# Optimization experiments

Measured on AMD Instinct MI355X. Metric: run time of the kernel, lower is better.

Reference implementation:

```python
import jax, jax.numpy as jnp
import numpy as np

B, N, K, E, H, V = 128, 256, 4, 300, 150, 32000  # batch, nodes/tree, max children, embed, hidden, vocab
DELTA = 1.0


def setup_inputs() -> dict:
    key = jax.random.key(0)
    ks = jax.random.split(key, 8)
    query = jax.random.randint(ks[0], (B, N), 0, V, dtype=jnp.int32)
    pos = jax.random.randint(ks[1], (B, N), 0, V, dtype=jnp.int32)
    neg = jax.random.randint(ks[2], (B, N), 0, V, dtype=jnp.int32)
    # Complete K-ary tree over N nodes: children of node t are {K*t+1, ..., K*t+K} < N; root = node 0.
    ch = np.full((N, K), -1, dtype=np.int32)
    for t in range(N):
        for j in range(K):
            c = K * t + 1 + j
            if c < N:
                ch[t, j] = c
    children = jnp.asarray(ch)
    emb = jax.random.normal(ks[3], (V, E), dtype=jnp.float32) * 0.02
    W_iou = jax.random.normal(ks[4], (E, 3 * H), dtype=jnp.float32) * 0.05
    U_iou = jax.random.normal(ks[5], (H, 3 * H), dtype=jnp.float32) * 0.05
    b_iou = jnp.zeros((3 * H,), jnp.float32)
    W_f = jax.random.normal(ks[6], (E, H), dtype=jnp.float32) * 0.05
    U_f = jax.random.normal(ks[7], (H, H), dtype=jnp.float32) * 0.05
    b_f = jnp.zeros((H,), jnp.float32)
    return {"query": query, "pos": pos, "neg": neg, "children": children,
            "emb": emb, "W_iou": W_iou, "U_iou": U_iou, "b_iou": b_iou,
            "W_f": W_f, "U_f": U_f, "b_f": b_f}


def _childsum_treelstm(x, children, W_iou, U_iou, b_iou, W_f, U_f, b_f):
    """x: [B, N, E] node embeddings. Returns root (c, h): each [B, H]."""
    Bn, Nn, _ = x.shape
    Hh = U_f.shape[0]
    h0 = jnp.zeros((Bn, Nn, Hh), x.dtype)
    c0 = jnp.zeros((Bn, Nn, Hh), x.dtype)

    def step(carry, t):
        h_all, c_all = carry
        ch = children[t]                        # [K] child indices, -1 = padding
        mask = (ch >= 0)
        idx = jnp.where(mask, ch, 0)
        m = mask.astype(x.dtype)[None, :, None]  # [1, K, 1]
        h_k = h_all[:, idx] * m                 # [B, K, H]
        c_k = c_all[:, idx] * m
        h_sum = h_k.sum(axis=1)                 # child-sum h_tilde [B, H]
        x_t = x[:, t]                           # [B, E]
        iou = x_t @ W_iou + h_sum @ U_iou + b_iou
        i, o, u = jnp.split(iou, 3, axis=-1)
        i = jax.nn.sigmoid(i)
        o = jax.nn.sigmoid(o)
        u = jnp.tanh(u)
        # per-child forget gates: f_jk = sigmoid(W_f x_j + U_f h_k + b_f)
        f = jax.nn.sigmoid((x_t @ W_f + b_f)[:, None, :] + h_k @ U_f)  # [B, K, H]
        c_t = i * u + (f * c_k).sum(axis=1)     # c_k already masked
        h_t = o * jnp.tanh(c_t)
        return (h_all.at[:, t].set(h_t), c_all.at[:, t].set(c_t)), None

    # children have larger indices than parents -> process N-1 .. 0 (root last)
    (h_all, c_all), _ = jax.lax.scan(step, (h0, c0), jnp.arange(Nn - 1, -1, -1))
    return c_all[:, 0], h_all[:, 0]


def _cosine(a, b):
    num = (a * b).sum(-1)
    den = jnp.sqrt((a * a).sum(-1) * (b * b).sum(-1)) + 1e-8
    return num / den


def reference(query, pos, neg, children, emb, W_iou, U_iou, b_iou, W_f, U_f, b_f):
    qc, _ = _childsum_treelstm(emb[query], children, W_iou, U_iou, b_iou, W_f, U_f, b_f)
    pc, _ = _childsum_treelstm(emb[pos], children, W_iou, U_iou, b_iou, W_f, U_f, b_f)
    nc, _ = _childsum_treelstm(emb[neg], children, W_iou, U_iou, b_iou, W_f, U_f, b_f)
    a = _cosine(qc, pc)  # [B]
    b = _cosine(qc, nc)  # [B]
    return jax.nn.relu(DELTA - a + b)
```

## Files before the change

### kernel.cpp

```cpp
#include <hip/hip_runtime.h>
#include <hip/hip_bf16.h>

typedef short short8 __attribute__((ext_vector_type(8)));
typedef float floatx4 __attribute__((ext_vector_type(4)));
typedef unsigned short ushort;

#define Bb 128
#define Nn 256
#define Hh 150
#define HK 160
#define Vv 32000
#define NROW 384
#define PROJC 600
#define NINT 64
#define ZROW (Vv + NROW * NINT)

__device__ __forceinline__ float sigf(float x) { return 1.0f / (1.0f + __expf(-x)); }
__device__ __forceinline__ float tanhf_(float x) { return 1.0f - 2.0f / (__expf(2.0f * x) + 1.0f); }
__device__ __forceinline__ float bf2f(ushort s) { union { float f; unsigned u; } v; v.u = ((unsigned)s) << 16; return v.f; }
__device__ __forceinline__ ushort f2bf(float f) { __hip_bfloat16 h = __float2bfloat16(f); return *(ushort*)&h; }

__global__ __launch_bounds__(256) void k_prep(
    const float* __restrict__ W_iou, const float* __restrict__ W_f,
    const float* __restrict__ U_iou, const float* __restrict__ U_f,
    const float* __restrict__ b_iou, const float* __restrict__ b_f,
    short* __restrict__ Wt, short* __restrict__ Uti, short* __restrict__ Utf,
    float* __restrict__ biasw, ushort* __restrict__ h_u, float* __restrict__ c_u)
{
    int idx = blockIdx.x * 256 + threadIdx.x;
    const int nWt = 608 * 320, nUi = 464 * 160, nUf = 160 * 160;
    if (idx < nWt) {
        int n = idx / 320, k = idx % 320;
        float v = 0.f;
        if (k < 300) { if (n < 450) v = W_iou[k * 450 + n]; else if (n < 600) v = W_f[k * 150 + (n - 450)]; }
        Wt[idx] = (short)f2bf(v);
    } else if (idx < nWt + nUi) {
        int i2 = idx - nWt; int n = i2 / 160, k = i2 % 160;
        float v = (k < 150 && n < 450) ? U_iou[k * 450 + n] : 0.f;
        Uti[i2] = (short)f2bf(v);
    } else if (idx < nWt + nUi + nUf) {
        int i2 = idx - nWt - nUi; int n = i2 / 160, k = i2 % 160;
        float v = (k < 150) ? U_f[k * 150 + n] : 0.f;
        Utf[i2] = (short)f2bf(v);
    } else if (idx < nWt + nUi + nUf + 608) {
        int n = idx - nWt - nUi - nUf;
        biasw[n] = n < 450 ? b_iou[n] : (n < 600 ? b_f[n - 450] : 0.f);
    } else if (idx < nWt + nUi + nUf + 608 + HK) {
        int k = idx - (nWt + nUi + nUf + 608);
        h_u[(long)ZROW * HK + k] = 0;
        c_u[(long)ZROW * HK + k] = 0.f;
    }
}

__global__ __launch_bounds__(256) void k_vproj(
    const float* __restrict__ emb, const short* __restrict__ Wt,
    const float* __restrict__ biasw, ushort* __restrict__ proj)
{
    __shared__ __align__(16) short As[32 * 328];
    const int tid = threadIdx.x;
    const int v0 = blockIdx.x * 32;

    for (int i = tid; i < 32 * 80; i += 256) {
        int r = i / 80, q = i % 80, k0 = q * 4;
        short4 sv;
        if (k0 < 300) {
            float4 x = *(const float4*)(emb + (long)(v0 + r) * 300 + k0);
            sv.x = (short)f2bf(x.x); sv.y = (short)f2bf(x.y);
            sv.z = (short)f2bf(x.z); sv.w = (short)f2bf(x.w);
        } else sv = make_short4(0, 0, 0, 0);
        *(short4*)&As[r * 328 + k0] = sv;
    }
    __syncthreads();

    const int w = tid >> 6, lane = tid & 63;
    const int m = lane & 15, kq = (lane >> 4) * 8;

    short8 a0[10], a1[10];
    #pragma unroll
    for (int ks = 0; ks < 10; ks++) {
        a0[ks] = *(const short8*)&As[m * 328 + kq + ks * 32];
        a1[ks] = *(const short8*)&As[(16 + m) * 328 + kq + ks * 32];
    }

    for (int nt = w; nt < 38; nt += 4) {
        int col = nt * 16 + m;
        const short* bp = Wt + (long)col * 320 + kq;
        floatx4 acc0 = {0.f, 0.f, 0.f, 0.f}, acc1 = {0.f, 0.f, 0.f, 0.f};
        #pragma unroll
        for (int ks = 0; ks < 10; ks++) {
            short8 b = *(const short8*)(bp + ks * 32);
            acc0 = __builtin_amdgcn_mfma_f32_16x16x32_bf16(a0[ks], b, acc0, 0, 0, 0);
            acc1 = __builtin_amdgcn_mfma_f32_16x16x32_bf16(a1[ks], b, acc1, 0, 0, 0);
        }
        if (col < PROJC) {
            float bias = biasw[col];
            int rb = (lane >> 4) * 4;
            #pragma unroll
            for (int reg = 0; reg < 4; reg++) {
                proj[(long)(v0 + rb + reg) * PROJC + col]      = f2bf(acc0[reg] + bias);
                proj[(long)(v0 + 16 + rb + reg) * PROJC + col] = f2bf(acc1[reg] + bias);
            }
        }
    }
}

__global__ __launch_bounds__(256) void k_vleaf(
    const ushort* __restrict__ proj, ushort* __restrict__ h_u, float* __restrict__ c_u)
{
    int idx = blockIdx.x * 256 + threadIdx.x;
    int v = idx / 20, k0 = (idx % 20) * 8;
    const ushort* pr = proj + (long)v * PROJC;
    ushort hv[8]; float cvv[8];
    #pragma unroll
    for (int e = 0; e < 8; e++) {
        int k = k0 + e;
        if (k < Hh) {
            float iv = sigf(bf2f(pr[k]));
            float ov = sigf(bf2f(pr[150 + k]));
            float uv = tanhf_(bf2f(pr[300 + k]));
            float cc = iv * uv;
            cvv[e] = cc;
            hv[e] = f2bf(ov * tanhf_(cc));
        } else { cvv[e] = 0.f; hv[e] = 0; }
    }
    *(int4*)(h_u + (long)v * HK + k0) = *(int4*)hv;
    *(float4*)(c_u + (long)v * HK + k0)     = make_float4(cvv[0], cvv[1], cvv[2], cvv[3]);
    *(float4*)(c_u + (long)v * HK + k0 + 4) = make_float4(cvv[4], cvv[5], cvv[6], cvv[7]);
}

__global__ __launch_bounds__(256) void k_level(
    int t0,
    const int* __restrict__ tq, const int* __restrict__ tp, const int* __restrict__ tn,
    const int* __restrict__ children, const ushort* __restrict__ proj,
    const short* __restrict__ Uti, const short* __restrict__ Utf,
    ushort* __restrict__ h_u, float* __restrict__ c_u)
{
    __shared__ __align__(16) short As[5][16][168];
    __shared__ int idx_s[16][4];
    __shared__ int tok_s[16];

    const int tid = threadIdx.x;
    const int t = t0 + blockIdx.x / 24;
    const int r0 = (blockIdx.x % 24) * 16;

    if (tid < 64) {
        int r = tid >> 2, j = tid & 3;
        int rg = r0 + r, g = rg >> 7, b = rg & 127;
        const int* tok = (g == 0) ? tq : (g == 1 ? tp : tn);
        int ch = children[t * 4 + j];
        int idx;
        if (ch < 0)        idx = ZROW;
        else if (ch >= 64) idx = tok[b * Nn + ch];
        else               idx = Vv + rg * NINT + ch;
        idx_s[r][j] = idx;
        if (j == 0) tok_s[r] = tok[b * Nn + t];
    }
    __syncthreads();

    for (int i = tid; i < 16 * 20; i += 256) {
        int r = i / 20, k0 = (i % 20) * 8;
        int4 v0 = *(const int4*)(h_u + (long)idx_s[r][0] * HK + k0);
        int4 v1 = *(const int4*)(h_u + (long)idx_s[r][1] * HK + k0);
        int4 v2 = *(const int4*)(h_u + (long)idx_s[r][2] * HK + k0);
        int4 v3 = *(const int4*)(h_u + (long)idx_s[r][3] * HK + k0);
        *(int4*)&As[1][r][k0] = v0;
        *(int4*)&As[2][r][k0] = v1;
        *(int4*)&As[3][r][k0] = v2;
        *(int4*)&As[4][r][k0] = v3;
        ushort s[8];
        const ushort* p0 = (const ushort*)&v0; const ushort* p1 = (const ushort*)&v1;
        const ushort* p2 = (const ushort*)&v2; const ushort* p3 = (const ushort*)&v3;
        #pragma unroll
        for (int e = 0; e < 8; e++)
            s[e] = f2bf(bf2f(p0[e]) + bf2f(p1[e]) + bf2f(p2[e]) + bf2f(p3[e]));
        *(int4*)&As[0][r][k0] = *(int4*)s;
    }
    __syncthreads();

    const int w = tid >> 6, lane = tid & 63;
    const int m = lane & 15, kq = (lane >> 4) * 8;

    for (int nt = w; nt < 10; nt += 4) {
        int col = nt * 16 + m;
        const short* bi  = Uti + (long)(col) * HK + kq;
        const short* bo  = Uti + (long)(150 + col) * HK + kq;
        const short* bu  = Uti + (long)(300 + col) * HK + kq;
        const short* bff = Utf + (long)col * HK + kq;
        floatx4 ai = {0.f,0.f,0.f,0.f}, ao = ai, au = ai;
        floatx4 af0 = ai, af1 = ai, af2 = ai, af3 = ai;
        #pragma unroll
        for (int ks = 0; ks < 5; ks++) {
            short8 asum = *(const short8*)&As[0][m][kq + ks * 32];
            short8 ac0  = *(const short8*)&As[1][m][kq + ks * 32];
            short8 ac1  = *(const short8*)&As[2][m][kq + ks * 32];
            short8 ac2  = *(const short8*)&As[3][m][kq + ks * 32];
            short8 ac3  = *(const short8*)&As[4][m][kq + ks * 32];
            short8 vbi = *(const short8*)(bi + ks * 32);
            short8 vbo = *(const short8*)(bo + ks * 32);
            short8 vbu = *(const short8*)(bu + ks * 32);
            short8 vbf = *(const short8*)(bff + ks * 32);
            ai  = __builtin_amdgcn_mfma_f32_16x16x32_bf16(asum, vbi, ai, 0, 0, 0);
            ao  = __builtin_amdgcn_mfma_f32_16x16x32_bf16(asum, vbo, ao, 0, 0, 0);
            au  = __builtin_amdgcn_mfma_f32_16x16x32_bf16(asum, vbu, au, 0, 0, 0);
            af0 = __builtin_amdgcn_mfma_f32_16x16x32_bf16(ac0,  vbf, af0, 0, 0, 0);
            af1 = __builtin_amdgcn_mfma_f32_16x16x32_bf16(ac1,  vbf, af1, 0, 0, 0);
            af2 = __builtin_amdgcn_mfma_f32_16x16x32_bf16(ac2,  vbf, af2, 0, 0, 0);
            af3 = __builtin_amdgcn_mfma_f32_16x16x32_bf16(ac3,  vbf, af3, 0, 0, 0);
        }

        int rbase = (lane >> 4) * 4;
        if (col < Hh) {
            #pragma unroll
            for (int reg = 0; reg < 4; reg++) {
                int r = rbase + reg, rg = r0 + r;
                const ushort* pr = proj + (long)tok_s[r] * PROJC;
                float iv = sigf(bf2f(pr[col])        + ai[reg]);
                float ov = sigf(bf2f(pr[150 + col])  + ao[reg]);
                float uv = tanhf_(bf2f(pr[300 + col]) + au[reg]);
                float fpre = bf2f(pr[450 + col]);
                float cv = iv * uv;
                cv = fmaf(sigf(fpre + af0[reg]), c_u[(long)idx_s[r][0] * HK + col], cv);
                cv = fmaf(sigf(fpre + af1[reg]), c_u[(long)idx_s[r][1] * HK + col], cv);
                cv = fmaf(sigf(fpre + af2[reg]), c_u[(long)idx_s[r][2] * HK + col], cv);
                cv = fmaf(sigf(fpre + af3[reg]), c_u[(long)idx_s[r][3] * HK + col], cv);
                long o = (long)(Vv + rg * NINT + t) * HK + col;
                c_u[o] = cv;
                h_u[o] = f2bf(ov * tanhf_(cv));
            }
        } else {
            #pragma unroll
            for (int reg = 0; reg < 4; reg++) {
                long o = (long)(Vv + (r0 + rbase + reg) * NINT + t) * HK + col;
                c_u[o] = 0.f; h_u[o] = 0;
            }
        }
    }
}

__global__ __launch_bounds__(64) void k_cos(const float* __restrict__ c_u, float* __restrict__ out)
{
    int b = blockIdx.x, tid = threadIdx.x;
    const float* qc = c_u + (long)(Vv + (0 * Bb + b) * NINT) * HK;
    const float* pc = c_u + (long)(Vv + (1 * Bb + b) * NINT) * HK;
    const float* nc = c_u + (long)(Vv + (2 * Bb + b) * NINT) * HK;
    float qp = 0, qn = 0, qq = 0, pp = 0, nn2 = 0;
    for (int k = tid; k < Hh; k += 64) {
        float qv = qc[k], pv = pc[k], nv = nc[k];
        qp += qv * pv; qn += qv * nv; qq += qv * qv; pp += pv * pv; nn2 += nv * nv;
    }
    #pragma unroll
    for (int off = 32; off > 0; off >>= 1) {
        qp += __shfl_down(qp, off, 64);
        qn += __shfl_down(qn, off, 64);
        qq += __shfl_down(qq, off, 64);
        pp += __shfl_down(pp, off, 64);
        nn2 += __shfl_down(nn2, off, 64);
    }
    if (tid == 0) {
        float a = qp / (sqrtf(qq * pp) + 1e-8f);
        float d = qn / (sqrtf(qq * nn2) + 1e-8f);
        out[b] = fmaxf(0.0f, 1.0f - a + d);
    }
}

extern "C" void kernel_launch(void* const* d_in, const int* in_sizes, int n_in,
                              void* d_out, int out_size, void* d_ws, size_t ws_size,
                              hipStream_t stream)
{
    const int*   tq       = (const int*)d_in[0];
    const int*   tp       = (const int*)d_in[1];
    const int*   tn       = (const int*)d_in[2];
    const int*   children = (const int*)d_in[3];
    const float* emb      = (const float*)d_in[4];
    const float* W_iou    = (const float*)d_in[5];
    const float* U_iou    = (const float*)d_in[6];
    const float* b_iou    = (const float*)d_in[7];
    const float* W_f      = (const float*)d_in[8];
    const float* U_f      = (const float*)d_in[9];
    const float* b_f      = (const float*)d_in[10];
    float* out = (float*)d_out;

    char* ws = (char*)d_ws;
    ushort* proj  = (ushort*)ws;
    ushort* h_u   = (ushort*)(ws + 38400000);
    float*  c_u   = (float*)(ws + 56504640);
    short*  Wt    = (short*)(ws + 92713920);
    short*  Uti   = (short*)(ws + 93103040);
    short*  Utf   = (short*)(ws + 93251520);
    float*  biasw = (float*)(ws + 93302720);

    k_prep<<<1153, 256, 0, stream>>>(W_iou, W_f, U_iou, U_f, b_iou, b_f,
                                     Wt, Uti, Utf, biasw, h_u, c_u);
    k_vproj<<<Vv / 32, 256, 0, stream>>>(emb, Wt, biasw, proj);
    k_vleaf<<<2500, 256, 0, stream>>>(proj, h_u, c_u);
    k_level<<<43 * 24, 256, 0, stream>>>(21, tq, tp, tn, children, proj, Uti, Utf, h_u, c_u);
    k_level<<<16 * 24, 256, 0, stream>>>(5,  tq, tp, tn, children, proj, Uti, Utf, h_u, c_u);
    k_level<<<4 * 24, 256, 0, stream>>>(1,   tq, tp, tn, children, proj, Uti, Utf, h_u, c_u);
    k_level<<<1 * 24, 256, 0, stream>>>(0,   tq, tp, tn, children, proj, Uti, Utf, h_u, c_u);
    k_cos<<<Bb, 64, 0, stream>>>(c_u, out);
}
```

Baseline: 272.3 us.

## Restructure vocab projection GEMM to keep weights in registers with double-buffered rows

Each k_vproj block now owns one 64-column slice of the weight matrix, held in registers, and walks 320 embedding rows in 10 chunks of 32. The next chunk's fp32 embeddings are prefetched into registers and converted into a second LDS buffer while the current chunk runs MFMAs. Previously every block reloaded all 38 weight column tiles from global memory for only 32 rows. The cost is that the emb rows are read 10 times (once per column group) instead of once, plus more registers per thread and a padded weight buffer of 640 columns.

```diff
diff --git a/kernel.cpp b/kernel.cpp
--- a/kernel.cpp
+++ b/kernel.cpp
@@ -15,6 +15,8 @@
 #define NINT 64
 #define ZROW (Vv + NROW * NINT)
 
+#define WTN 640
+
 __device__ __forceinline__ float sigf(float x) { return 1.0f / (1.0f + __expf(-x)); }
 __device__ __forceinline__ float tanhf_(float x) { return 1.0f - 2.0f / (__expf(2.0f * x) + 1.0f); }
 __device__ __forceinline__ float bf2f(ushort s) { union { float f; unsigned u; } v; v.u = ((unsigned)s) << 16; return v.f; }
@@ -28,7 +30,7 @@
     float* __restrict__ biasw, ushort* __restrict__ h_u, float* __restrict__ c_u)
 {
     int idx = blockIdx.x * 256 + threadIdx.x;
-    const int nWt = 608 * 320, nUi = 464 * 160, nUf = 160 * 160;
+    const int nWt = WTN * 320, nUi = 464 * 160, nUf = 160 * 160;
     if (idx < nWt) {
         int n = idx / 320, k = idx % 320;
         float v = 0.f;
@@ -42,11 +44,11 @@
         int i2 = idx - nWt - nUi; int n = i2 / 160, k = i2 % 160;
         float v = (k < 150) ? U_f[k * 150 + n] : 0.f;
         Utf[i2] = (short)f2bf(v);
-    } else if (idx < nWt + nUi + nUf + 608) {
+    } else if (idx < nWt + nUi + nUf + WTN) {
         int n = idx - nWt - nUi - nUf;
         biasw[n] = n < 450 ? b_iou[n] : (n < 600 ? b_f[n - 450] : 0.f);
-    } else if (idx < nWt + nUi + nUf + 608 + HK) {
-        int k = idx - (nWt + nUi + nUf + 608);
+    } else if (idx < nWt + nUi + nUf + WTN + HK) {
+        int k = idx - (nWt + nUi + nUf + WTN);
         h_u[(long)ZROW * HK + k] = 0;
         c_u[(long)ZROW * HK + k] = 0.f;
     }
@@ -56,44 +58,65 @@
     const float* __restrict__ emb, const short* __restrict__ Wt,
     const float* __restrict__ biasw, ushort* __restrict__ proj)
 {
-    __shared__ __align__(16) short As[32 * 328];
+    __shared__ __align__(16) short As[2][32][328];
     const int tid = threadIdx.x;
-    const int v0 = blockIdx.x * 32;
-
-    for (int i = tid; i < 32 * 80; i += 256) {
-        int r = i / 80, q = i % 80, k0 = q * 4;
-        short4 sv;
-        if (k0 < 300) {
-            float4 x = *(const float4*)(emb + (long)(v0 + r) * 300 + k0);
+    const int cg = blockIdx.x % 10;
+    const int rg = blockIdx.x / 10;
+    const int rowbase = rg * 320;
+
+    const int w = tid >> 6, lane = tid & 63;
+    const int m = lane & 15, kq = (lane >> 4) * 8;
+    const int tile = cg * 4 + w;
+    const int col = tile * 16 + m;
+
+    short8 bq[10];
+    #pragma unroll
+    for (int ks = 0; ks < 10; ks++)
+        bq[ks] = *(const short8*)(Wt + (long)col * 320 + kq + ks * 32);
+    const float bias = biasw[col];
+
+    for (int i = tid; i < 2 * 32 * 5; i += 256) {
+        int bz = i / 160, r2 = (i % 160) / 5, kk = (i % 5) * 4;
+        *(short4*)&As[bz][r2][300 + kk] = make_short4(0, 0, 0, 0);
+    }
+
+    {
+        const float4* src = (const float4*)emb + (long)rowbase * 75;
+        for (int i = tid; i < 2400; i += 256) {
+            int r = i / 75, k0 = (i % 75) * 4;
+            float4 x = src[i];
+            short4 sv;
             sv.x = (short)f2bf(x.x); sv.y = (short)f2bf(x.y);
             sv.z = (short)f2bf(x.z); sv.w = (short)f2bf(x.w);
-        } else sv = make_short4(0, 0, 0, 0);
-        *(short4*)&As[r * 328 + k0] = sv;
+            *(short4*)&As[0][r][k0] = sv;
+        }
     }
     __syncthreads();
 
-    const int w = tid >> 6, lane = tid & 63;
-    const int m = lane & 15, kq = (lane >> 4) * 8;
-
-    short8 a0[10], a1[10];
-    #pragma unroll
-    for (int ks = 0; ks < 10; ks++) {
-        a0[ks] = *(const short8*)&As[m * 328 + kq + ks * 32];
-        a1[ks] = *(const short8*)&As[(16 + m) * 328 + kq + ks * 32];
-    }
-
-    for (int nt = w; nt < 38; nt += 4) {
-        int col = nt * 16 + m;
-        const short* bp = Wt + (long)col * 320 + kq;
+    for (int c = 0; c < 10; c++) {
+        const int buf = c & 1;
+
+        float4 x[10];
+        if (c < 9) {
+            const float4* src = (const float4*)emb + (long)(rowbase + (c + 1) * 32) * 75;
+            #pragma unroll
+            for (int j = 0; j < 10; j++) {
+                int i = tid + j * 256;
+                if (i < 2400) x[j] = src[i];
+            }
+        }
+
         floatx4 acc0 = {0.f, 0.f, 0.f, 0.f}, acc1 = {0.f, 0.f, 0.f, 0.f};
         #pragma unroll
         for (int ks = 0; ks < 10; ks++) {
-            short8 b = *(const short8*)(bp + ks * 32);
-            acc0 = __builtin_amdgcn_mfma_f32_16x16x32_bf16(a0[ks], b, acc0, 0, 0, 0);
-            acc1 = __builtin_amdgcn_mfma_f32_16x16x32_bf16(a1[ks], b, acc1, 0, 0, 0);
-        }
+            short8 a0 = *(const short8*)&As[buf][m][kq + ks * 32];
+            short8 a1 = *(const short8*)&As[buf][16 + m][kq + ks * 32];
+            acc0 = __builtin_amdgcn_mfma_f32_16x16x32_bf16(a0, bq[ks], acc0, 0, 0, 0);
+            acc1 = __builtin_amdgcn_mfma_f32_16x16x32_bf16(a1, bq[ks], acc1, 0, 0, 0);
+        }
+
         if (col < PROJC) {
-            float bias = biasw[col];
+            int v0 = rowbase + c * 32;
             int rb = (lane >> 4) * 4;
             #pragma unroll
             for (int reg = 0; reg < 4; reg++) {
@@ -101,6 +124,21 @@
                 proj[(long)(v0 + 16 + rb + reg) * PROJC + col] = f2bf(acc1[reg] + bias);
             }
         }
+
+        if (c < 9) {
+            #pragma unroll
+            for (int j = 0; j < 10; j++) {
+                int i = tid + j * 256;
+                if (i < 2400) {
+                    int r = i / 75, k0 = (i % 75) * 4;
+                    short4 sv;
+                    sv.x = (short)f2bf(x[j].x); sv.y = (short)f2bf(x[j].y);
+                    sv.z = (short)f2bf(x[j].z); sv.w = (short)f2bf(x[j].w);
+                    *(short4*)&As[buf ^ 1][r][k0] = sv;
+                }
+            }
+        }
+        __syncthreads();
     }
 }
 
@@ -285,13 +323,13 @@
     ushort* h_u   = (ushort*)(ws + 38400000);
     float*  c_u   = (float*)(ws + 56504640);
     short*  Wt    = (short*)(ws + 92713920);
-    short*  Uti   = (short*)(ws + 93103040);
-    short*  Utf   = (short*)(ws + 93251520);
-    float*  biasw = (float*)(ws + 93302720);
-
-    k_prep<<<1153, 256, 0, stream>>>(W_iou, W_f, U_iou, U_f, b_iou, b_f,
+    short*  Uti   = (short*)(ws + 93123520);
+    short*  Utf   = (short*)(ws + 93272000);
+    float*  biasw = (float*)(ws + 93323200);
+
+    k_prep<<<1194, 256, 0, stream>>>(W_iou, W_f, U_iou, U_f, b_iou, b_f,
                                      Wt, Uti, Utf, biasw, h_u, c_u);
-    k_vproj<<<Vv / 32, 256, 0, stream>>>(emb, Wt, biasw, proj);
+    k_vproj<<<1000, 256, 0, stream>>>(emb, Wt, biasw, proj);
     k_vleaf<<<2500, 256, 0, stream>>>(proj, h_u, c_u);
     k_level<<<43 * 24, 256, 0, stream>>>(21, tq, tp, tn, children, proj, Uti, Utf, h_u, c_u);
     k_level<<<16 * 24, 256, 0, stream>>>(5,  tq, tp, tn, children, proj, Uti, Utf, h_u, c_u);
```

After: 270.8 us. About the same (-0.6%).
